# Performance work log

Measured on AMD Instinct MI355X. Metric: run time of the kernel, lower is better.

The kernel has to match this reference:

```python
import jax, jax.numpy as jnp
import numpy as np

N_U = 50000
N_I = 50000
E = 800000
HID = 64
HEADS = 4
OUT = 32
NEG_SLOPE = 0.2


def _gat(xs, xd, e, ws, wd, a_s, a_d, b, heads, ch, n_dst, concat):
    # xs:[Ns,Fin] xd:[Nd,Fin] e:[2,E]; PyG GATConv (no self loops, eval mode)
    hs = (xs @ ws).reshape(-1, heads, ch)  # [Ns,H,C]
    hd = (xd @ wd).reshape(-1, heads, ch)  # [Nd,H,C]
    al_s = jnp.einsum('nhc,hc->nh', hs, a_s)  # [Ns,H]
    al_d = jnp.einsum('nhc,hc->nh', hd, a_d)  # [Nd,H]
    src, dst = e[0], e[1]
    alpha = jax.nn.leaky_relu(al_s[src] + al_d[dst], NEG_SLOPE)  # [E,H]
    m = jax.lax.stop_gradient(jax.ops.segment_max(alpha, dst, num_segments=n_dst))
    ealpha = jnp.exp(alpha - m[dst])
    denom = jax.ops.segment_sum(ealpha, dst, num_segments=n_dst)
    coef = ealpha / (denom[dst] + 1e-16)  # segment softmax over incoming edges
    msg = hs[src] * coef[:, :, None]  # [E,H,C]
    out = jax.ops.segment_sum(msg, dst, num_segments=n_dst)  # [Nd,H,C]
    out = out.reshape(n_dst, heads * ch) if concat else out.mean(axis=1)
    return out + b


def _forward(x_user, x_item, e_u2i, e_i2u,
             p_user_w, p_user_b, p_item_w, p_item_b,
             l0_u2i_ws, l0_u2i_wd, l0_u2i_as, l0_u2i_ad, l0_u2i_b,
             l0_i2u_ws, l0_i2u_wd, l0_i2u_as, l0_i2u_ad, l0_i2u_b,
             l1_u2i_ws, l1_u2i_wd, l1_u2i_as, l1_u2i_ad, l1_u2i_b,
             l1_i2u_ws, l1_i2u_wd, l1_i2u_as, l1_i2u_ad, l1_i2u_b):
    hu = jax.nn.elu(x_user @ p_user_w + p_user_b)
    hi = jax.nn.elu(x_item @ p_item_w + p_item_b)
    # layer 0: heads=4, concat=True, out dim HID*HEADS; HeteroConv sum (one edge type per dst)
    hi1 = _gat(hu, hi, e_u2i, l0_u2i_ws, l0_u2i_wd, l0_u2i_as, l0_u2i_ad, l0_u2i_b, HEADS, HID, N_I, True)
    hu1 = _gat(hi, hu, e_i2u, l0_i2u_ws, l0_i2u_wd, l0_i2u_as, l0_i2u_ad, l0_i2u_b, HEADS, HID, N_U, True)
    hu1 = jax.nn.elu(hu1)  # dropout is identity in eval mode
    hi1 = jax.nn.elu(hi1)
    # layer 1: heads=1, concat=False -> mean over heads
    hi2 = _gat(hu1, hi1, e_u2i, l1_u2i_ws, l1_u2i_wd, l1_u2i_as, l1_u2i_ad, l1_u2i_b, 1, OUT, N_I, False)
    hu2 = _gat(hi1, hu1, e_i2u, l1_i2u_ws, l1_i2u_wd, l1_i2u_as, l1_i2u_ad, l1_i2u_b, 1, OUT, N_U, False)
    return hu2, hi2


def setup_inputs() -> dict:
    key = jax.random.key(0)
    ks = jax.random.split(key, 32)
    s = 0.1
    d = {
        'x_user': jax.random.normal(ks[0], (N_U, 128), jnp.float32),
        'x_item': jax.random.normal(ks[1], (N_I, 128), jnp.float32),
        'e_u2i': jax.random.randint(ks[2], (2, E), 0, 50000, jnp.int32),
        'e_i2u': jax.random.randint(ks[3], (2, E), 0, 50000, jnp.int32),
        'p_user_w': jax.random.normal(ks[4], (128, HID), jnp.float32) * s,
        'p_user_b': jax.random.normal(ks[5], (HID,), jnp.float32) * s,
        'p_item_w': jax.random.normal(ks[6], (128, HID), jnp.float32) * s,
        'p_item_b': jax.random.normal(ks[7], (HID,), jnp.float32) * s,
    }
    i = 8
    for lname, fin, h, c in (('l0', HID, HEADS, HID), ('l1', HID * HEADS, 1, OUT)):
        for et in ('u2i', 'i2u'):
            odim = h * c if lname == 'l0' else c
            d[f'{lname}_{et}_ws'] = jax.random.normal(ks[i], (fin, h * c), jnp.float32) * s; i += 1
            d[f'{lname}_{et}_wd'] = jax.random.normal(ks[i], (fin, h * c), jnp.float32) * s; i += 1
            d[f'{lname}_{et}_as'] = jax.random.normal(ks[i], (h, c), jnp.float32) * s; i += 1
            d[f'{lname}_{et}_ad'] = jax.random.normal(ks[i], (h, c), jnp.float32) * s; i += 1
            d[f'{lname}_{et}_b'] = jax.random.normal(ks[i], (odim,), jnp.float32) * s; i += 1
    return d


def reference(x_user, x_item, e_u2i, e_i2u,
              p_user_w, p_user_b, p_item_w, p_item_b,
              l0_u2i_ws, l0_u2i_wd, l0_u2i_as, l0_u2i_ad, l0_u2i_b,
              l0_i2u_ws, l0_i2u_wd, l0_i2u_as, l0_i2u_ad, l0_i2u_b,
              l1_u2i_ws, l1_u2i_wd, l1_u2i_as, l1_u2i_ad, l1_u2i_b,
              l1_i2u_ws, l1_i2u_wd, l1_i2u_as, l1_i2u_ad, l1_i2u_b):
    return _forward(x_user, x_item, e_u2i, e_i2u,
                    p_user_w, p_user_b, p_item_w, p_item_b,
                    l0_u2i_ws, l0_u2i_wd, l0_u2i_as, l0_u2i_ad, l0_u2i_b,
                    l0_i2u_ws, l0_i2u_wd, l0_i2u_as, l0_i2u_ad, l0_i2u_b,
                    l1_u2i_ws, l1_u2i_wd, l1_u2i_as, l1_u2i_ad, l1_u2i_b,
                    l1_i2u_ws, l1_i2u_wd, l1_i2u_as, l1_i2u_ad, l1_i2u_b)
```

## Files before the change

### kernel.cpp

```cpp
#include <hip/hip_runtime.h>
#include <cstdint>
#include <cstddef>

#define NN 50000
#define NE 800000
#define GB 196
#define TILE1 4096
#define CAP 8192

typedef __attribute__((ext_vector_type(8))) short short8;
typedef __attribute__((ext_vector_type(4))) float floatx4;

__device__ __forceinline__ float lrelu_f(float x){ return x >= 0.f ? x : 0.2f*x; }
__device__ __forceinline__ float elu_f(float x){ return x > 0.f ? x : __expf(x) - 1.f; }

__device__ __forceinline__ unsigned short f2bf(float f){
  unsigned int u = __float_as_uint(f);
  u += 0x7FFFu + ((u >> 16) & 1u);
  return (unsigned short)(u >> 16);
}
__device__ __forceinline__ float bf2f(unsigned int us){
  return __uint_as_float(us << 16);
}
__device__ __forceinline__ float4 bf4_load(const unsigned short* p){
  uint2 q = *(const uint2*)p;
  return make_float4(bf2f(q.x & 0xffffu), bf2f(q.x >> 16),
                     bf2f(q.y & 0xffffu), bf2f(q.y >> 16));
}
__device__ __forceinline__ uint2 bf4_pack(float4 o){
  uint2 p;
  p.x = (unsigned)f2bf(o.x) | ((unsigned)f2bf(o.y) << 16);
  p.y = (unsigned)f2bf(o.z) | ((unsigned)f2bf(o.w) << 16);
  return p;
}
__device__ __forceinline__ void split_bf(float a, unsigned short& h, unsigned short& l){
  h = f2bf(a);
  l = f2bf(a - bf2f(h));
}

__global__ __launch_bounds__(256) void ghist_kernel(const int* __restrict__ e0,
                                                    const int* __restrict__ e1,
                                                    int* __restrict__ ghist){
  const int ty = blockIdx.y;
  const int* e = ty ? e1 : e0;
  __shared__ int h[GB];
  for (int j=threadIdx.x; j<GB; j+=256) h[j]=0;
  __syncthreads();
  for (int i = blockIdx.x*256 + threadIdx.x; i < NE; i += 256*256)
    atomicAdd(&h[e[NE+i]>>8], 1);
  __syncthreads();
  for (int j=threadIdx.x; j<GB; j+=256) if (h[j]) atomicAdd(&ghist[ty*200+j], h[j]);
}

__global__ __launch_bounds__(256) void gscan_kernel(const int* __restrict__ ghist,
                                                    int* __restrict__ gbase,
                                                    int* __restrict__ gcur){
  __shared__ int wb[4];
  const int t = threadIdx.x, wv = t>>6, l = t&63;
  for (int ty=0; ty<2; ++ty){
    int v = (t < GB) ? ghist[ty*200+t] : 0;
    int sum = v;
    #pragma unroll
    for (int off=1; off<64; off<<=1){
      int x = __shfl_up(sum, off, 64);
      if (l >= off) sum += x;
    }
    if (l == 63) wb[wv] = sum;
    __syncthreads();
    int wbase = 0;
    #pragma unroll
    for (int w=0; w<4; ++w) if (w < wv) wbase += wb[w];
    int excl = wbase + sum - v;
    if (t <= GB) gbase[ty*200+t] = excl;
    if (t <  GB) gcur [ty*200+t] = excl;
    __syncthreads();
  }
}

__global__ __launch_bounds__(256) void part1_kernel(const int* __restrict__ e0,
                                                    const int* __restrict__ e1,
                                                    int* __restrict__ gcur,
                                                    int2* __restrict__ p0,
                                                    int2* __restrict__ p1){
  const int ty = blockIdx.y;
  const int* e = ty ? e1 : e0;
  int2* pairs = ty ? p1 : p0;
  __shared__ int cnt[256];
  __shared__ int lstart[256];
  __shared__ int lcur[256];
  __shared__ int curg[GB];
  __shared__ int lsrc[TILE1];
  __shared__ int ldst[TILE1];
  __shared__ int wb[4];
  const int t = threadIdx.x;
  cnt[t] = 0;
  __syncthreads();
  int dreg[16], sreg[16];
  const int base = blockIdx.x*TILE1;
  const int ntile = min(TILE1, NE - base);
  #pragma unroll
  for (int it=0; it<16; ++it){
    int i = base + it*256 + t;
    int d = -1, s = 0;
    if (i < NE){ d = e[NE+i]; s = e[i]; atomicAdd(&cnt[d>>8], 1); }
    dreg[it] = d; sreg[it] = s;
  }
  __syncthreads();
  int c = cnt[t], sum = c;
  #pragma unroll
  for (int off=1; off<64; off<<=1){
    int x = __shfl_up(sum, off, 64);
    if ((t&63) >= off) sum += x;
  }
  if ((t&63) == 63) wb[t>>6] = sum;
  __syncthreads();
  int wbase = 0;
  #pragma unroll
  for (int w=0; w<4; ++w) if (w < (t>>6)) wbase += wb[w];
  int excl = wbase + sum - c;
  lstart[t] = excl;
  lcur[t] = excl;
  if (t < GB && c > 0) curg[t] = atomicAdd(&gcur[ty*200+t], c);
  __syncthreads();
  #pragma unroll
  for (int it=0; it<16; ++it){
    int d = dreg[it];
    if (d >= 0){
      int pos = atomicAdd(&lcur[d>>8], 1);
      lsrc[pos] = sreg[it];
      ldst[pos] = d;
    }
  }
  __syncthreads();
  for (int i=t; i<ntile; i+=256){
    int d = ldst[i];
    int j = d>>8;
    pairs[curg[j] + (i - lstart[j])] = make_int2(lsrc[i], d);
  }
}

struct Part2Job {
  const int2* pairs; const int* gbase;
  const float* als; const float* ald;
  int* ssrc; int* offs; unsigned short* coef;
};
__global__ __launch_bounds__(256) void part2_kernel(Part2Job j0, Part2Job j1){
  const Part2Job jb = blockIdx.y ? j1 : j0;
  const int b = blockIdx.x;
  const int t = threadIdx.x;
  __shared__ int lcnt[256];
  __shared__ int lcur[256];
  __shared__ int wb[4];
  __shared__ int sorted_src[CAP];
  __shared__ unsigned char sorted_dl[CAP];
  const int gb0 = jb.gbase[b], gb1 = jb.gbase[b+1];
  const int n = gb1 - gb0;
  lcnt[t] = 0;
  __syncthreads();
  for (int i=t; i<n; i+=256)
    atomicAdd(&lcnt[jb.pairs[gb0+i].y - (b<<8)], 1);
  __syncthreads();
  int c = lcnt[t], sum = c;
  #pragma unroll
  for (int off=1; off<64; off<<=1){
    int x = __shfl_up(sum, off, 64);
    if ((t&63) >= off) sum += x;
  }
  if ((t&63) == 63) wb[t>>6] = sum;
  __syncthreads();
  int wbase = 0;
  #pragma unroll
  for (int w=0; w<4; ++w) if (w < (t>>6)) wbase += wb[w];
  int excl = wbase + sum - c;
  lcur[t] = excl;
  int g = (b<<8) + t;
  if (g <= NN) jb.offs[g] = gb0 + excl;
  __syncthreads();
  for (int i=t; i<n; i+=256){
    int2 pr = jb.pairs[gb0+i];
    int dl = pr.y - (b<<8);
    int pos = atomicAdd(&lcur[dl], 1);
    sorted_src[pos] = pr.x;
    sorted_dl[pos] = (unsigned char)dl;
  }
  __syncthreads();
  const float4* als4 = (const float4*)jb.als;
  const float4* ald4 = (const float4*)jb.ald;
  for (int i=t; i<n; i+=256){
    int s  = sorted_src[i];
    int dl = sorted_dl[i];
    float4 a  = als4[s];
    float4 ad = ald4[(b<<8)+dl];
    float4 w;
    w.x = __expf(lrelu_f(a.x+ad.x));
    w.y = __expf(lrelu_f(a.y+ad.y));
    w.z = __expf(lrelu_f(a.z+ad.z));
    w.w = __expf(lrelu_f(a.w+ad.w));
    ((uint2*)jb.coef)[gb0+i] = bf4_pack(w);
    jb.ssrc[gb0+i] = s;
  }
}

struct MgJob {
  const void* A; const float* W; const float* bias;
  void* C; float* outA; float* outB;
  const float* cwS; const float* cwD;
};
template<int NT, bool ELU, bool BF16OUT, bool BF16A, bool LG, bool LOGIT>
__global__ __launch_bounds__(256) void mgemm_kernel(MgJob j0, MgJob j1,
                                                    int M, int K, int N)
{
  const MgJob jb = blockIdx.z ? j1 : j0;
  constexpr int TN = NT*16;
  __shared__ __align__(16) unsigned short Ah[64*72];
  __shared__ __align__(16) unsigned short Al[BF16A ? 8 : 64*72];
  __shared__ __align__(16) unsigned short Bh[TN*72];
  __shared__ __align__(16) unsigned short Bl[TN*72];
  __shared__ float CwS[LOGIT ? 256 : 1];
  __shared__ float CwD[LOGIT ? 256 : 1];
  const int t = threadIdx.x;
  const int m0 = blockIdx.x*64;
  const int n0 = blockIdx.y*TN;
  const int wv = t>>6, l = t&63;
  const int lr = l&15, lq = l>>4;
  if constexpr (LOGIT){ CwS[t] = jb.cwS[t]; CwD[t] = jb.cwD[t]; }
  floatx4 acc[NT];
  #pragma unroll
  for (int i=0;i<NT;i++) acc[i] = (floatx4){0.f,0.f,0.f,0.f};

  for (int kt=0; kt<K; kt+=64){
    if constexpr (BF16A){
      const unsigned short* A = (const unsigned short*)jb.A;
      #pragma unroll
      for (int i=0;i<2;i++){
        int li = t + i*256;
        int r = li >> 3, c8 = (li & 7)*8;
        short8 v = {0,0,0,0,0,0,0,0};
        if (m0 + r < M) v = *(const short8*)(A + (size_t)(m0+r)*K + kt + c8);
        *(short8*)&Ah[r*72 + c8] = v;
      }
    } else {
      const float* A = (const float*)jb.A;
      #pragma unroll
      for (int i=0;i<4;i++){
        int li = t + i*256;
        int r = li >> 4, c4 = (li & 15)*4;
        float4 v = make_float4(0.f,0.f,0.f,0.f);
        if (m0 + r < M) v = *(const float4*)(A + (size_t)(m0+r)*K + kt + c4);
        unsigned short h0,h1,h2,h3,g0,g1,g2,g3;
        split_bf(v.x,h0,g0); split_bf(v.y,h1,g1);
        split_bf(v.z,h2,g2); split_bf(v.w,h3,g3);
        uint2 ph = { (unsigned)h0 | ((unsigned)h1<<16), (unsigned)h2 | ((unsigned)h3<<16) };
        uint2 pl = { (unsigned)g0 | ((unsigned)g1<<16), (unsigned)g2 | ((unsigned)g3<<16) };
        *(uint2*)&Ah[r*72 + c4] = ph;
        *(uint2*)&Al[r*72 + c4] = pl;
      }
    }
    #pragma unroll
    for (int i=0;i<NT;i++){
      int li = t + i*256;
      int k  = li / (TN/4);
      int n4 = (li % (TN/4))*4;
      float4 v = *(const float4*)(jb.W + (size_t)(kt+k)*N + n0 + n4);
      unsigned short h, g;
      split_bf(v.x,h,g); Bh[(n4+0)*72+k]=h; Bl[(n4+0)*72+k]=g;
      split_bf(v.y,h,g); Bh[(n4+1)*72+k]=h; Bl[(n4+1)*72+k]=g;
      split_bf(v.z,h,g); Bh[(n4+2)*72+k]=h; Bl[(n4+2)*72+k]=g;
      split_bf(v.w,h,g); Bh[(n4+3)*72+k]=h; Bl[(n4+3)*72+k]=g;
    }
    __syncthreads();
    #pragma unroll
    for (int ks=0; ks<2; ks++){
      const int koff = ks*32 + lq*8;
      short8 a_h = *(const short8*)&Ah[(wv*16+lr)*72 + koff];
      short8 a_l;
      if constexpr (!BF16A) a_l = *(const short8*)&Al[(wv*16+lr)*72 + koff];
      #pragma unroll
      for (int nt=0; nt<NT; nt++){
        short8 b_h = *(const short8*)&Bh[(nt*16+lr)*72 + koff];
        short8 b_l = *(const short8*)&Bl[(nt*16+lr)*72 + koff];
        acc[nt] = __builtin_amdgcn_mfma_f32_16x16x32_bf16(a_h, b_h, acc[nt], 0,0,0);
        acc[nt] = __builtin_amdgcn_mfma_f32_16x16x32_bf16(a_h, b_l, acc[nt], 0,0,0);
        if constexpr (!BF16A)
          acc[nt] = __builtin_amdgcn_mfma_f32_16x16x32_bf16(a_l, b_h, acc[nt], 0,0,0);
      }
    }
    __syncthreads();
  }
  float ls[LOGIT ? 4 : 1][LOGIT ? 4 : 1];
  float ld_[LOGIT ? 4 : 1][LOGIT ? 4 : 1];
  if constexpr (LOGIT){
    #pragma unroll
    for (int r=0;r<4;r++)
      #pragma unroll
      for (int h=0;h<4;h++){ ls[r][h]=0.f; ld_[r][h]=0.f; }
  }
  #pragma unroll
  for (int nt=0; nt<NT; nt++){
    int n = n0 + nt*16 + lr;
    float bv = jb.bias ? jb.bias[n] : 0.f;
    #pragma unroll
    for (int r=0;r<4;r++){
      int m = m0 + wv*16 + lq*4 + r;
      if (m < M){
        float o = acc[nt][r] + bv;
        if (ELU) o = elu_f(o);
        if constexpr (LG){
          if (n < 32)       ((unsigned short*)jb.C)[(size_t)m*32 + n] = f2bf(o);
          else if (n == 32) jb.outA[m] = o;
          else if (n == 33) jb.outB[m] = o;
        } else {
          if (BF16OUT) ((unsigned short*)jb.C)[(size_t)m*N + n] = f2bf(o);
          else         ((float*)jb.C)[(size_t)m*N + n] = o;
        }
        if constexpr (LOGIT){
          #pragma unroll
          for (int h=0;h<4;h++){
            ls[r][h]  = fmaf(o, CwS[h*64 + n], ls[r][h]);
            ld_[r][h] = fmaf(o, CwD[h*64 + n], ld_[r][h]);
          }
        }
      }
    }
  }
  if constexpr (LOGIT){
    #pragma unroll
    for (int r=0;r<4;r++)
      #pragma unroll
      for (int h=0;h<4;h++){
        float a = ls[r][h], d = ld_[r][h];
        #pragma unroll
        for (int off=1; off<16; off<<=1){
          a += __shfl_xor(a, off, 64);
          d += __shfl_xor(d, off, 64);
        }
        ls[r][h]=a; ld_[r][h]=d;
      }
    if (lr == 0){
      #pragma unroll
      for (int r=0;r<4;r++){
        int m = m0 + wv*16 + lq*4 + r;
        if (m < M){
          #pragma unroll
          for (int h=0;h<4;h++){
            jb.outA[(size_t)m*4 + h] = ls[r][h];
            jb.outB[(size_t)m*4 + h] = ld_[r][h];
          }
        }
      }
    }
  }
}

struct HgJob {
  const unsigned short* A; const float* W; const float* den;
  const float* bias; unsigned short* out;
};
__global__ __launch_bounds__(256) void hgemm_kernel(HgJob j0, HgJob j1){
  const HgJob jb = blockIdx.z ? j1 : j0;
  const int head = blockIdx.y;
  const int m0 = blockIdx.x*64;
  __shared__ __align__(16) unsigned short Ah[64*72];
  __shared__ __align__(16) unsigned short Bh[64*72];
  __shared__ __align__(16) unsigned short Bl[64*72];
  const int t = threadIdx.x;
  const int wv = t>>6, l = t&63;
  const int lr = l&15, lq = l>>4;
  floatx4 acc[4];
  #pragma unroll
  for (int i=0;i<4;i++) acc[i] = (floatx4){0.f,0.f,0.f,0.f};
  #pragma unroll
  for (int i=0;i<2;i++){
    int li = t + i*256;
    int r = li >> 3, c8 = (li & 7)*8;
    short8 v = {0,0,0,0,0,0,0,0};
    if (m0 + r < NN) v = *(const short8*)(jb.A + (size_t)(m0+r)*256 + head*64 + c8);
    *(short8*)&Ah[r*72 + c8] = v;
  }
  #pragma unroll
  for (int i=0;i<4;i++){
    int li = t + i*256;
    int k  = li >> 4;
    int n4 = (li & 15)*4;
    float4 v = *(const float4*)(jb.W + (size_t)k*256 + head*64 + n4);
    unsigned short h, g;
    split_bf(v.x,h,g); Bh[(n4+0)*72+k]=h; Bl[(n4+0)*72+k]=g;
    split_bf(v.y,h,g); Bh[(n4+1)*72+k]=h; Bl[(n4+1)*72+k]=g;
    split_bf(v.z,h,g); Bh[(n4+2)*72+k]=h; Bl[(n4+2)*72+k]=g;
    split_bf(v.w,h,g); Bh[(n4+3)*72+k]=h; Bl[(n4+3)*72+k]=g;
  }
  __syncthreads();
  #pragma unroll
  for (int ks=0; ks<2; ks++){
    const int koff = ks*32 + lq*8;
    short8 a_h = *(const short8*)&Ah[(wv*16+lr)*72 + koff];
    #pragma unroll
    for (int nt=0; nt<4; nt++){
      short8 b_h = *(const short8*)&Bh[(nt*16+lr)*72 + koff];
      short8 b_l = *(const short8*)&Bl[(nt*16+lr)*72 + koff];
      acc[nt] = __builtin_amdgcn_mfma_f32_16x16x32_bf16(a_h, b_h, acc[nt], 0,0,0);
      acc[nt] = __builtin_amdgcn_mfma_f32_16x16x32_bf16(a_h, b_l, acc[nt], 0,0,0);
    }
  }
  float inv[4];
  #pragma unroll
  for (int r=0;r<4;r++){
    int m = m0 + wv*16 + lq*4 + r;
    inv[r] = (m < NN) ? 1.f/(jb.den[(size_t)m*4 + head] + 1e-16f) : 0.f;
  }
  #pragma unroll
  for (int nt=0; nt<4; nt++){
    int col = head*64 + nt*16 + lr;
    float bv = jb.bias[col];
    #pragma unroll
    for (int r=0;r<4;r++){
      int m = m0 + wv*16 + lq*4 + r;
      if (m < NN)
        jb.out[(size_t)m*256 + col] = f2bf(elu_f(acc[nt][r]*inv[r] + bv));
    }
  }
}

struct CollapseJob { const float* W; const float* a; float* out; int K,H,C; };
struct CollapseArgs { CollapseJob j[8]; };
__global__ void collapse_kernel(CollapseArgs args){
  CollapseJob jb = args.j[blockIdx.x];
  int t = threadIdx.x;
  if (t < jb.K * jb.H){
    int k = t / jb.H, h = t % jb.H;
    const float* wr = jb.W + (size_t)k * (jb.H*jb.C) + h*jb.C;
    const float* ar = jb.a + h*jb.C;
    float s = 0.f;
    for (int c=0;c<jb.C;c++) s += wr[c]*ar[c];
    jb.out[h*jb.K + k] = s;
  }
}

__global__ __launch_bounds__(256) void prep1_kernel(
    const float* __restrict__ WsA, const float* __restrict__ cwSA, const float* __restrict__ cwDA,
    const float* __restrict__ WsB, const float* __restrict__ cwSB, const float* __restrict__ cwDB,
    float* __restrict__ WcA, float* __restrict__ WcB){
  const float* Ws  = blockIdx.x ? WsB  : WsA;
  const float* cwS = blockIdx.x ? cwSB : cwSA;
  const float* cwD = blockIdx.x ? cwDB : cwDA;
  float* Wc = blockIdx.x ? WcB : WcA;
  const int k = threadIdx.x;
  #pragma unroll
  for (int n=0;n<32;n++) Wc[(size_t)k*48 + n] = Ws[(size_t)k*32 + n];
  Wc[(size_t)k*48 + 32] = cwS[k];
  Wc[(size_t)k*48 + 33] = cwD[k];
  #pragma unroll
  for (int n=34;n<48;n++) Wc[(size_t)k*48 + n] = 0.f;
}

struct AggPJob {
  const int* offs; const int* ssrc;
  const unsigned short* x;
  const unsigned short* coef;
  unsigned short* agg;
  float* den;
};
__global__ __launch_bounds__(256) void aggpre_kernel(AggPJob ja, AggPJob jbb){
  const AggPJob jb = blockIdx.y ? jbb : ja;
  const int wid = threadIdx.x>>6, lane = threadIdx.x&63;
  const int dst = blockIdx.x*4 + wid;
  if (dst >= NN) return;
  const int b0 = jb.offs[dst], b1 = jb.offs[dst+1];
  const int g  = lane >> 4;
  const int c4 = (lane & 15)*4;
  float acc[4][4];
  float den[4] = {0.f,0.f,0.f,0.f};
  #pragma unroll
  for (int h=0;h<4;h++){ acc[h][0]=0.f; acc[h][1]=0.f; acc[h][2]=0.f; acc[h][3]=0.f; }
  int e = b0 + g;
  for (; e+4 < b1; e += 8){
    int s0 = jb.ssrc[e];
    int s1 = jb.ssrc[e+4];
    float4 xv0 = bf4_load(jb.x + ((size_t)s0<<6) + c4);
    float4 xv1 = bf4_load(jb.x + ((size_t)s1<<6) + c4);
    float4 wv0 = bf4_load(jb.coef + (size_t)e*4);
    float4 wv1 = bf4_load(jb.coef + (size_t)(e+4)*4);
    acc[0][0]+=wv0.x*xv0.x+wv1.x*xv1.x; acc[0][1]+=wv0.x*xv0.y+wv1.x*xv1.y;
    acc[0][2]+=wv0.x*xv0.z+wv1.x*xv1.z; acc[0][3]+=wv0.x*xv0.w+wv1.x*xv1.w;
    acc[1][0]+=wv0.y*xv0.x+wv1.y*xv1.x; acc[1][1]+=wv0.y*xv0.y+wv1.y*xv1.y;
    acc[1][2]+=wv0.y*xv0.z+wv1.y*xv1.z; acc[1][3]+=wv0.y*xv0.w+wv1.y*xv1.w;
    acc[2][0]+=wv0.z*xv0.x+wv1.z*xv1.x; acc[2][1]+=wv0.z*xv0.y+wv1.z*xv1.y;
    acc[2][2]+=wv0.z*xv0.z+wv1.z*xv1.z; acc[2][3]+=wv0.z*xv0.w+wv1.z*xv1.w;
    acc[3][0]+=wv0.w*xv0.x+wv1.w*xv1.x; acc[3][1]+=wv0.w*xv0.y+wv1.w*xv1.y;
    acc[3][2]+=wv0.w*xv0.z+wv1.w*xv1.z; acc[3][3]+=wv0.w*xv0.w+wv1.w*xv1.w;
    den[0]+=wv0.x+wv1.x; den[1]+=wv0.y+wv1.y; den[2]+=wv0.z+wv1.z; den[3]+=wv0.w+wv1.w;
  }
  if (e < b1){
    int s = jb.ssrc[e];
    float4 xv = bf4_load(jb.x + ((size_t)s<<6) + c4);
    float4 wv = bf4_load(jb.coef + (size_t)e*4);
    acc[0][0]+=wv.x*xv.x; acc[0][1]+=wv.x*xv.y; acc[0][2]+=wv.x*xv.z; acc[0][3]+=wv.x*xv.w;
    acc[1][0]+=wv.y*xv.x; acc[1][1]+=wv.y*xv.y; acc[1][2]+=wv.y*xv.z; acc[1][3]+=wv.y*xv.w;
    acc[2][0]+=wv.z*xv.x; acc[2][1]+=wv.z*xv.y; acc[2][2]+=wv.z*xv.z; acc[2][3]+=wv.z*xv.w;
    acc[3][0]+=wv.w*xv.x; acc[3][1]+=wv.w*xv.y; acc[3][2]+=wv.w*xv.z; acc[3][3]+=wv.w*xv.w;
    den[0]+=wv.x; den[1]+=wv.y; den[2]+=wv.z; den[3]+=wv.w;
  }
  #pragma unroll
  for (int off=16; off<=32; off<<=1){
    #pragma unroll
    for (int h=0;h<4;h++){
      acc[h][0] += __shfl_xor(acc[h][0], off, 64);
      acc[h][1] += __shfl_xor(acc[h][1], off, 64);
      acc[h][2] += __shfl_xor(acc[h][2], off, 64);
      acc[h][3] += __shfl_xor(acc[h][3], off, 64);
      den[h]    += __shfl_xor(den[h],    off, 64);
    }
  }
  if (lane < 16){
    #pragma unroll
    for (int h=0;h<4;h++){
      float4 o = make_float4(acc[h][0], acc[h][1], acc[h][2], acc[h][3]);
      *(uint2*)(jb.agg + (size_t)dst*256 + h*64 + c4) = bf4_pack(o);
    }
    if (lane == 0)
      *(float4*)(jb.den + (size_t)dst*4) = make_float4(den[0],den[1],den[2],den[3]);
  }
}

struct Agg1Job {
  const int* offs; const int* ssrc;
  const unsigned short* hs;
  const float* als; const float* ald;
  const float* bias; float* out;
};
__global__ __launch_bounds__(256) void agg1_kernel(Agg1Job ja, Agg1Job jbb){
  const Agg1Job jb = blockIdx.y ? jbb : ja;
  const int wid = threadIdx.x>>6, lane = threadIdx.x&63;
  const int dst = blockIdx.x*4 + wid;
  if (dst >= NN) return;
  const int b0 = jb.offs[dst], b1 = jb.offs[dst+1];
  const float ad = jb.ald[dst];
  const int slot = lane>>3, c4 = (lane&7)*4;
  float4 acc = make_float4(0.f,0.f,0.f,0.f);
  float den = 0.f;
  int e = b0 + slot;
  for (; e+8 < b1; e += 16){
    int s0 = jb.ssrc[e], s1 = jb.ssrc[e+8];
    float a0 = jb.als[s0];
    float a1 = jb.als[s1];
    float4 v0 = bf4_load(jb.hs + ((size_t)s0<<5) + c4);
    float4 v1 = bf4_load(jb.hs + ((size_t)s1<<5) + c4);
    float w0 = __expf(lrelu_f(a0 + ad));
    float w1 = __expf(lrelu_f(a1 + ad));
    acc.x += w0*v0.x + w1*v1.x;
    acc.y += w0*v0.y + w1*v1.y;
    acc.z += w0*v0.z + w1*v1.z;
    acc.w += w0*v0.w + w1*v1.w;
    den += w0 + w1;
  }
  if (e < b1){
    int s = jb.ssrc[e];
    float w = __expf(lrelu_f(jb.als[s] + ad));
    float4 v = bf4_load(jb.hs + ((size_t)s<<5) + c4);
    acc.x += w*v.x; acc.y += w*v.y; acc.z += w*v.z; acc.w += w*v.w;
    den += w;
  }
  #pragma unroll
  for (int off=32; off>=8; off>>=1){
    acc.x += __shfl_xor(acc.x, off, 64);
    acc.y += __shfl_xor(acc.y, off, 64);
    acc.z += __shfl_xor(acc.z, off, 64);
    acc.w += __shfl_xor(acc.w, off, 64);
    den   += __shfl_xor(den,   off, 64);
  }
  if (lane < 8){
    const float inv = 1.f/(den + 1e-16f);
    float4 b = *(const float4*)(jb.bias + c4);
    float4 o = make_float4(acc.x*inv+b.x, acc.y*inv+b.y, acc.z*inv+b.z, acc.w*inv+b.w);
    *(float4*)(jb.out + (size_t)dst*32 + c4) = o;
  }
}

extern "C" void kernel_launch(void* const* d_in, const int* in_sizes, int n_in,
                              void* d_out, int out_size, void* d_ws, size_t ws_size,
                              hipStream_t stream)
{
  (void)in_sizes; (void)n_in; (void)out_size; (void)ws_size;
  const float* x_user   = (const float*)d_in[0];
  const float* x_item   = (const float*)d_in[1];
  const int*   e_u2i    = (const int*)  d_in[2];
  const int*   e_i2u    = (const int*)  d_in[3];
  const float* p_user_w = (const float*)d_in[4];
  const float* p_user_b = (const float*)d_in[5];
  const float* p_item_w = (const float*)d_in[6];
  const float* p_item_b = (const float*)d_in[7];
  const float* l0_u2i_ws=(const float*)d_in[8];
  const float* l0_u2i_wd=(const float*)d_in[9];
  const float* l0_u2i_as=(const float*)d_in[10];
  const float* l0_u2i_ad=(const float*)d_in[11];
  const float* l0_u2i_b =(const float*)d_in[12];
  const float* l0_i2u_ws=(const float*)d_in[13];
  const float* l0_i2u_wd=(const float*)d_in[14];
  const float* l0_i2u_as=(const float*)d_in[15];
  const float* l0_i2u_ad=(const float*)d_in[16];
  const float* l0_i2u_b =(const float*)d_in[17];
  const float* l1_u2i_ws=(const float*)d_in[18];
  const float* l1_u2i_wd=(const float*)d_in[19];
  const float* l1_u2i_as=(const float*)d_in[20];
  const float* l1_u2i_ad=(const float*)d_in[21];
  const float* l1_u2i_b =(const float*)d_in[22];
  const float* l1_i2u_ws=(const float*)d_in[23];
  const float* l1_i2u_wd=(const float*)d_in[24];
  const float* l1_i2u_as=(const float*)d_in[25];
  const float* l1_i2u_ad=(const float*)d_in[26];
  const float* l1_i2u_b =(const float*)d_in[27];

  char* base = (char*)d_ws;
  size_t off = 0;
  auto alloc = [&](size_t bytes)->void*{
    void* p = base + off;
    off += (bytes + 255) & ~(size_t)255;
    return p;
  };
  int* offs_u2i = (int*)alloc((size_t)(NN+1)*sizeof(int));
  int* offs_i2u = (int*)alloc((size_t)(NN+1)*sizeof(int));
  int* ssrc_u2i = (int*)alloc((size_t)NE*sizeof(int));
  int* ssrc_i2u = (int*)alloc((size_t)NE*sizeof(int));
  int* ghist    = (int*)alloc((size_t)2*200*sizeof(int));
  int* gbase    = (int*)alloc((size_t)2*200*sizeof(int));
  int* gcur     = (int*)alloc((size_t)2*200*sizeof(int));
  unsigned short* coef0_u2i = (unsigned short*)alloc((size_t)NE*4*sizeof(unsigned short));
  unsigned short* coef0_i2u = (unsigned short*)alloc((size_t)NE*4*sizeof(unsigned short));
  unsigned short* hu = (unsigned short*)alloc((size_t)NN*64*sizeof(unsigned short));
  unsigned short* hi = (unsigned short*)alloc((size_t)NN*64*sizeof(unsigned short));
  unsigned short* agg_u2i = (unsigned short*)alloc((size_t)NN*256*sizeof(unsigned short));
  unsigned short* agg_i2u = (unsigned short*)alloc((size_t)NN*256*sizeof(unsigned short));
  float* den_u2i = (float*)alloc((size_t)NN*4*sizeof(float));
  float* den_i2u = (float*)alloc((size_t)NN*4*sizeof(float));
  unsigned short* hu1 = (unsigned short*)alloc((size_t)NN*256*sizeof(unsigned short));
  unsigned short* hi1 = (unsigned short*)alloc((size_t)NN*256*sizeof(unsigned short));
  unsigned short* hs1_u2i = (unsigned short*)alloc((size_t)NN*32*sizeof(unsigned short));
  unsigned short* hs1_i2u = (unsigned short*)alloc((size_t)NN*32*sizeof(unsigned short));
  float* als0_u2i = (float*)alloc((size_t)NN*4*sizeof(float));
  float* ald0_u2i = (float*)alloc((size_t)NN*4*sizeof(float));
  float* als0_i2u = (float*)alloc((size_t)NN*4*sizeof(float));
  float* ald0_i2u = (float*)alloc((size_t)NN*4*sizeof(float));
  float* als1_u2i = (float*)alloc((size_t)NN*sizeof(float));
  float* ald1_u2i = (float*)alloc((size_t)NN*sizeof(float));
  float* als1_i2u = (float*)alloc((size_t)NN*sizeof(float));
  float* ald1_i2u = (float*)alloc((size_t)NN*sizeof(float));
  float* cw0s_u2i = (float*)alloc(256*sizeof(float));
  float* cw0d_u2i = (float*)alloc(256*sizeof(float));
  float* cw0s_i2u = (float*)alloc(256*sizeof(float));
  float* cw0d_i2u = (float*)alloc(256*sizeof(float));
  float* cw1s_u2i = (float*)alloc(256*sizeof(float));
  float* cw1d_u2i = (float*)alloc(256*sizeof(float));
  float* cw1s_i2u = (float*)alloc(256*sizeof(float));
  float* cw1d_i2u = (float*)alloc(256*sizeof(float));
  float* Wc_u2i   = (float*)alloc((size_t)256*48*sizeof(float));
  float* Wc_i2u   = (float*)alloc((size_t)256*48*sizeof(float));
  int2* pairs_u2i = (int2*)hu1;
  int2* pairs_i2u = pairs_u2i + NE;

  const int GM = (NN + 63)/64;

  hipMemsetAsync(ghist, 0, (size_t)2*200*sizeof(int), stream);
  ghist_kernel<<<dim3(256,2), 256, 0, stream>>>(e_u2i, e_i2u, ghist);
  gscan_kernel<<<1, 256, 0, stream>>>(ghist, gbase, gcur);
  part1_kernel<<<dim3((NE+TILE1-1)/TILE1,2), 256, 0, stream>>>(
      e_u2i, e_i2u, gcur, pairs_u2i, pairs_i2u);

  CollapseArgs ca;
  ca.j[0] = {l0_u2i_ws, l0_u2i_as, cw0s_u2i, 64, 4, 64};
  ca.j[1] = {l0_u2i_wd, l0_u2i_ad, cw0d_u2i, 64, 4, 64};
  ca.j[2] = {l0_i2u_ws, l0_i2u_as, cw0s_i2u, 64, 4, 64};
  ca.j[3] = {l0_i2u_wd, l0_i2u_ad, cw0d_i2u, 64, 4, 64};
  ca.j[4] = {l1_u2i_ws, l1_u2i_as, cw1s_u2i, 256, 1, 32};
  ca.j[5] = {l1_u2i_wd, l1_u2i_ad, cw1d_u2i, 256, 1, 32};
  ca.j[6] = {l1_i2u_ws, l1_i2u_as, cw1s_i2u, 256, 1, 32};
  ca.j[7] = {l1_i2u_wd, l1_i2u_ad, cw1d_i2u, 256, 1, 32};
  collapse_kernel<<<8, 256, 0, stream>>>(ca);

  mgemm_kernel<4,true,true,false,false,true><<<dim3(GM,1,2), 256, 0, stream>>>(
      MgJob{x_user, p_user_w, p_user_b, hu, als0_u2i, ald0_i2u, cw0s_u2i, cw0d_i2u},
      MgJob{x_item, p_item_w, p_item_b, hi, als0_i2u, ald0_u2i, cw0s_i2u, cw0d_u2i},
      NN, 128, 64);

  prep1_kernel<<<2, 256, 0, stream>>>(
      l1_u2i_ws, cw1s_u2i, cw1d_i2u,
      l1_i2u_ws, cw1s_i2u, cw1d_u2i,
      Wc_u2i, Wc_i2u);

  part2_kernel<<<dim3(GB,2), 256, 0, stream>>>(
      Part2Job{pairs_u2i, gbase,       als0_u2i, ald0_u2i, ssrc_u2i, offs_u2i, coef0_u2i},
      Part2Job{pairs_i2u, gbase + 200, als0_i2u, ald0_i2u, ssrc_i2u, offs_i2u, coef0_i2u});

  aggpre_kernel<<<dim3(NN/4,2), 256, 0, stream>>>(
      AggPJob{offs_u2i, ssrc_u2i, hu, coef0_u2i, agg_u2i, den_u2i},
      AggPJob{offs_i2u, ssrc_i2u, hi, coef0_i2u, agg_i2u, den_i2u});

  hgemm_kernel<<<dim3(GM,4,2), 256, 0, stream>>>(
      HgJob{agg_u2i, l0_u2i_ws, den_u2i, l0_u2i_b, hi1},
      HgJob{agg_i2u, l0_i2u_ws, den_i2u, l0_i2u_b, hu1});

  mgemm_kernel<3,false,true,true,true,false><<<dim3(GM,1,2), 256, 0, stream>>>(
      MgJob{hu1, Wc_u2i, nullptr, hs1_u2i, als1_u2i, ald1_i2u, nullptr, nullptr},
      MgJob{hi1, Wc_i2u, nullptr, hs1_i2u, als1_i2u, ald1_u2i, nullptr, nullptr},
      NN, 256, 48);

  float* hu2 = (float*)d_out;
  float* hi2 = (float*)d_out + (size_t)NN*32;
  agg1_kernel<<<dim3(NN/4,2), 256, 0, stream>>>(
      Agg1Job{offs_u2i, ssrc_u2i, hs1_u2i, als1_u2i, ald1_u2i, l1_u2i_b, hi2},
      Agg1Job{offs_i2u, ssrc_i2u, hs1_i2u, als1_i2u, ald1_i2u, l1_i2u_b, hu2});
}
```

Measured before the change: 407.2 us.

## Remap aggpre to 8 lanes per destination and use bf16 dot2 accumulation

The pre-aggregation kernel now gives each destination node an 8-lane group instead of a full wavefront. Each lane loads 8 bf16 channels with one 16-byte load and walks every edge of its node, so the cross-lane shuffle reduction goes away. Pairs of edges are packed with byte permutes and accumulated with v_dot2_f32_bf16, which also computes the denominator via a dot with ones. This trades more serial edge work per lane and more accumulator registers for fewer idle lanes on low-degree nodes, fewer shuffles and fewer multiply-add instructions.

```diff
diff --git a/kernel.cpp b/kernel.cpp
--- a/kernel.cpp
+++ b/kernel.cpp
@@ -36,6 +36,11 @@
 __device__ __forceinline__ void split_bf(float a, unsigned short& h, unsigned short& l){
   h = f2bf(a);
   l = f2bf(a - bf2f(h));
+}
+
+__device__ __forceinline__ float dot2bf(float acc, unsigned a, unsigned b){
+  asm("v_dot2_f32_bf16 %0, %1, %2, %0" : "+v"(acc) : "v"(a), "v"(b));
+  return acc;
 }
 
 __global__ __launch_bounds__(256) void ghist_kernel(const int* __restrict__ e0,
@@ -462,64 +467,76 @@
 };
 __global__ __launch_bounds__(256) void aggpre_kernel(AggPJob ja, AggPJob jbb){
   const AggPJob jb = blockIdx.y ? jbb : ja;
-  const int wid = threadIdx.x>>6, lane = threadIdx.x&63;
-  const int dst = blockIdx.x*4 + wid;
+  const int tid = threadIdx.x;
+  const int lane = tid & 63, wid = tid >> 6;
+  const int grp = lane >> 3;
+  const int cl  = lane & 7;
+  const int c8  = cl * 8;
+  const int dst = blockIdx.x*32 + wid*8 + grp;
   if (dst >= NN) return;
   const int b0 = jb.offs[dst], b1 = jb.offs[dst+1];
-  const int g  = lane >> 4;
-  const int c4 = (lane & 15)*4;
-  float acc[4][4];
+  float acc[4][8];
   float den[4] = {0.f,0.f,0.f,0.f};
   #pragma unroll
-  for (int h=0;h<4;h++){ acc[h][0]=0.f; acc[h][1]=0.f; acc[h][2]=0.f; acc[h][3]=0.f; }
-  int e = b0 + g;
-  for (; e+4 < b1; e += 8){
+  for (int h=0;h<4;h++)
+    #pragma unroll
+    for (int c=0;c<8;c++) acc[h][c]=0.f;
+  const unsigned ONE2 = 0x3F803F80u;
+  int e = b0;
+  for (; e+1 < b1; e += 2){
     int s0 = jb.ssrc[e];
-    int s1 = jb.ssrc[e+4];
-    float4 xv0 = bf4_load(jb.x + ((size_t)s0<<6) + c4);
-    float4 xv1 = bf4_load(jb.x + ((size_t)s1<<6) + c4);
-    float4 wv0 = bf4_load(jb.coef + (size_t)e*4);
-    float4 wv1 = bf4_load(jb.coef + (size_t)(e+4)*4);
-    acc[0][0]+=wv0.x*xv0.x+wv1.x*xv1.x; acc[0][1]+=wv0.x*xv0.y+wv1.x*xv1.y;
-    acc[0][2]+=wv0.x*xv0.z+wv1.x*xv1.z; acc[0][3]+=wv0.x*xv0.w+wv1.x*xv1.w;
-    acc[1][0]+=wv0.y*xv0.x+wv1.y*xv1.x; acc[1][1]+=wv0.y*xv0.y+wv1.y*xv1.y;
-    acc[1][2]+=wv0.y*xv0.z+wv1.y*xv1.z; acc[1][3]+=wv0.y*xv0.w+wv1.y*xv1.w;
-    acc[2][0]+=wv0.z*xv0.x+wv1.z*xv1.x; acc[2][1]+=wv0.z*xv0.y+wv1.z*xv1.y;
-    acc[2][2]+=wv0.z*xv0.z+wv1.z*xv1.z; acc[2][3]+=wv0.z*xv0.w+wv1.z*xv1.w;
-    acc[3][0]+=wv0.w*xv0.x+wv1.w*xv1.x; acc[3][1]+=wv0.w*xv0.y+wv1.w*xv1.y;
-    acc[3][2]+=wv0.w*xv0.z+wv1.w*xv1.z; acc[3][3]+=wv0.w*xv0.w+wv1.w*xv1.w;
-    den[0]+=wv0.x+wv1.x; den[1]+=wv0.y+wv1.y; den[2]+=wv0.z+wv1.z; den[3]+=wv0.w+wv1.w;
+    int s1 = jb.ssrc[e+1];
+    uint4 q0 = *(const uint4*)(jb.x + ((size_t)s0<<6) + c8);
+    uint4 q1 = *(const uint4*)(jb.x + ((size_t)s1<<6) + c8);
+    uint2 w0 = *(const uint2*)(jb.coef + (size_t)e*4);
+    uint2 w1 = *(const uint2*)(jb.coef + (size_t)(e+1)*4);
+    unsigned wp[4];
+    wp[0] = __builtin_amdgcn_perm(w1.x, w0.x, 0x05040100u);
+    wp[1] = __builtin_amdgcn_perm(w1.x, w0.x, 0x07060302u);
+    wp[2] = __builtin_amdgcn_perm(w1.y, w0.y, 0x05040100u);
+    wp[3] = __builtin_amdgcn_perm(w1.y, w0.y, 0x07060302u);
+    unsigned xp[8];
+    xp[0] = __builtin_amdgcn_perm(q1.x, q0.x, 0x05040100u);
+    xp[1] = __builtin_amdgcn_perm(q1.x, q0.x, 0x07060302u);
+    xp[2] = __builtin_amdgcn_perm(q1.y, q0.y, 0x05040100u);
+    xp[3] = __builtin_amdgcn_perm(q1.y, q0.y, 0x07060302u);
+    xp[4] = __builtin_amdgcn_perm(q1.z, q0.z, 0x05040100u);
+    xp[5] = __builtin_amdgcn_perm(q1.z, q0.z, 0x07060302u);
+    xp[6] = __builtin_amdgcn_perm(q1.w, q0.w, 0x05040100u);
+    xp[7] = __builtin_amdgcn_perm(q1.w, q0.w, 0x07060302u);
+    #pragma unroll
+    for (int h=0;h<4;h++){
+      den[h] = dot2bf(den[h], wp[h], ONE2);
+      #pragma unroll
+      for (int c=0;c<8;c++) acc[h][c] = dot2bf(acc[h][c], wp[h], xp[c]);
+    }
   }
   if (e < b1){
     int s = jb.ssrc[e];
-    float4 xv = bf4_load(jb.x + ((size_t)s<<6) + c4);
-    float4 wv = bf4_load(jb.coef + (size_t)e*4);
-    acc[0][0]+=wv.x*xv.x; acc[0][1]+=wv.x*xv.y; acc[0][2]+=wv.x*xv.z; acc[0][3]+=wv.x*xv.w;
-    acc[1][0]+=wv.y*xv.x; acc[1][1]+=wv.y*xv.y; acc[1][2]+=wv.y*xv.z; acc[1][3]+=wv.y*xv.w;
-    acc[2][0]+=wv.z*xv.x; acc[2][1]+=wv.z*xv.y; acc[2][2]+=wv.z*xv.z; acc[2][3]+=wv.z*xv.w;
-    acc[3][0]+=wv.w*xv.x; acc[3][1]+=wv.w*xv.y; acc[3][2]+=wv.w*xv.z; acc[3][3]+=wv.w*xv.w;
-    den[0]+=wv.x; den[1]+=wv.y; den[2]+=wv.z; den[3]+=wv.w;
-  }
-  #pragma unroll
-  for (int off=16; off<=32; off<<=1){
+    uint4 q = *(const uint4*)(jb.x + ((size_t)s<<6) + c8);
+    uint2 w = *(const uint2*)(jb.coef + (size_t)e*4);
+    float wf[4] = { bf2f(w.x & 0xffffu), bf2f(w.x >> 16),
+                    bf2f(w.y & 0xffffu), bf2f(w.y >> 16) };
+    float xf[8] = { bf2f(q.x & 0xffffu), bf2f(q.x >> 16),
+                    bf2f(q.y & 0xffffu), bf2f(q.y >> 16),
+                    bf2f(q.z & 0xffffu), bf2f(q.z >> 16),
+                    bf2f(q.w & 0xffffu), bf2f(q.w >> 16) };
     #pragma unroll
     for (int h=0;h<4;h++){
-      acc[h][0] += __shfl_xor(acc[h][0], off, 64);
-      acc[h][1] += __shfl_xor(acc[h][1], off, 64);
-      acc[h][2] += __shfl_xor(acc[h][2], off, 64);
-      acc[h][3] += __shfl_xor(acc[h][3], off, 64);
-      den[h]    += __shfl_xor(den[h],    off, 64);
-    }
-  }
-  if (lane < 16){
-    #pragma unroll
-    for (int h=0;h<4;h++){
-      float4 o = make_float4(acc[h][0], acc[h][1], acc[h][2], acc[h][3]);
-      *(uint2*)(jb.agg + (size_t)dst*256 + h*64 + c4) = bf4_pack(o);
-    }
-    if (lane == 0)
-      *(float4*)(jb.den + (size_t)dst*4) = make_float4(den[0],den[1],den[2],den[3]);
-  }
+      den[h] += wf[h];
+      #pragma unroll
+      for (int c=0;c<8;c++) acc[h][c] += wf[h]*xf[c];
+    }
+  }
+  #pragma unroll
+  for (int h=0;h<4;h++){
+    uint2 plo = bf4_pack(make_float4(acc[h][0],acc[h][1],acc[h][2],acc[h][3]));
+    uint2 phi = bf4_pack(make_float4(acc[h][4],acc[h][5],acc[h][6],acc[h][7]));
+    uint4 pk = { plo.x, plo.y, phi.x, phi.y };
+    *(uint4*)(jb.agg + (size_t)dst*256 + h*64 + c8) = pk;
+  }
+  if (cl == 0)
+    *(float4*)(jb.den + (size_t)dst*4) = make_float4(den[0],den[1],den[2],den[3]);
 }
 
 struct Agg1Job {
@@ -690,7 +707,7 @@
       Part2Job{pairs_u2i, gbase,       als0_u2i, ald0_u2i, ssrc_u2i, offs_u2i, coef0_u2i},
       Part2Job{pairs_i2u, gbase + 200, als0_i2u, ald0_i2u, ssrc_i2u, offs_i2u, coef0_i2u});
 
-  aggpre_kernel<<<dim3(NN/4,2), 256, 0, stream>>>(
+  aggpre_kernel<<<dim3((NN+31)/32,2), 256, 0, stream>>>(
       AggPJob{offs_u2i, ssrc_u2i, hu, coef0_u2i, agg_u2i, den_u2i},
       AggPJob{offs_i2u, ssrc_i2u, hi, coef0_i2u, agg_i2u, den_i2u});
 
```

New measurement: 398.5 us. -2.1%, faster.
